# Optimization experiments

Hardware: AMD Instinct MI355X
Metric: run time of the kernel (lower is better)

## Reference

```python
import jax, jax.numpy as jnp
import numpy as np

N_EMBED = 1024
CUTOFFS = [20000, 60000, 180000]
N_VOCAB = 267735
BOUNDS = [0] + CUTOFFS + [N_VOCAB]            # cluster boundaries
N_EMBEDS = [1024, 256, 64, 16]                # n_embed / 4**i
N_TOK = 1024
N_CLUSTERS = len(CUTOFFS)                      # 3 tail clusters


def setup_inputs() -> dict:
    key = jax.random.key(0)
    ks = jax.random.split(key, 12)

    def w(k, shape):
        fan_in = shape[0]
        return (jax.random.normal(k, shape, jnp.float32) / np.sqrt(fan_in)).astype(jnp.float32)

    inp = {}
    inp["hidden"] = jax.random.normal(ks[0], (N_TOK, N_EMBED), jnp.float32)
    inp["target"] = jax.random.randint(ks[1], (N_TOK,), 0, N_VOCAB)
    # head: layers[0] = Linear(n_embed, cutoffs[0]); clusters = Linear(n_embed, n_clusters)
    inp["W_head"] = w(ks[2], (N_EMBED, BOUNDS[1]))
    inp["b_head"] = jnp.zeros((BOUNDS[1],), jnp.float32)
    inp["W_cluster"] = w(ks[3], (N_EMBED, N_CLUSTERS))
    inp["b_cluster"] = jnp.zeros((N_CLUSTERS,), jnp.float32)
    # tails: projections[i-1] = Linear(n_embed, n_embeds[i], bias=False); layers[i] = Linear(n_embeds[i], end-start)
    for i in range(1, N_CLUSTERS + 1):
        size = BOUNDS[i + 1] - BOUNDS[i]
        inp[f"W_proj{i}"] = w(ks[3 + 2 * i], (N_EMBED, N_EMBEDS[i]))
        inp[f"W_tail{i}"] = w(ks[4 + 2 * i], (N_EMBEDS[i], size))
        inp[f"b_tail{i}"] = jnp.zeros((size,), jnp.float32)
    return inp


def _adaptive_nll(hidden, target, W_head, b_head, W_cluster, b_cluster, tails):
    # head logits = [vocab cluster 0 | cluster logits], then log_softmax (matches torch.cat + log_softmax)
    head_logit = jnp.concatenate(
        [hidden @ W_head + b_head, hidden @ W_cluster + b_cluster], axis=1)  # [N, cut0 + n_clusters]
    head_lp = jax.nn.log_softmax(head_logit, axis=1)

    # cluster 0: logprob = head_lp[n, target]
    t0 = jnp.clip(target, 0, BOUNDS[1] - 1)
    lp0 = jnp.take_along_axis(head_lp, t0[:, None], axis=1)[:, 0]
    nll = jnp.where(target < BOUNDS[1], -lp0, jnp.zeros((), head_lp.dtype))

    # tail clusters i=1..3: logprob = head_lp[:, -i] + tail_log_softmax[n, target-start]
    for i, (Wp, Wt, bt) in enumerate(tails, start=1):
        start, end = BOUNDS[i], BOUNDS[i + 1]
        tail_lp = jax.nn.log_softmax((hidden @ Wp) @ Wt + bt, axis=1)  # [N, end-start]
        rel = jnp.clip(target - start, 0, end - start - 1)
        lp_i = head_lp[:, -i] + jnp.take_along_axis(tail_lp, rel[:, None], axis=1)[:, 0]
        in_bucket = (target >= start) & (target < end)
        nll = jnp.where(in_bucket, -lp_i, nll)
    return nll  # [N], per-token negative log-likelihood (keep_order=True semantics)


def reference(hidden, target, W_head, b_head, W_cluster, b_cluster,
              W_proj1, W_tail1, b_tail1,
              W_proj2, W_tail2, b_tail2,
              W_proj3, W_tail3, b_tail3):
    tails = [(W_proj1, W_tail1, b_tail1),
             (W_proj2, W_tail2, b_tail2),
             (W_proj3, W_tail3, b_tail3)]
    return _adaptive_nll(hidden, target, W_head, b_head, W_cluster, b_cluster, tails)
```

## Files before the change

kernel.cpp:

```cpp
#include <hip/hip_runtime.h>
#include <cstdint>
#include <cstddef>


typedef unsigned short u16;
typedef __attribute__((ext_vector_type(8))) __bf16 bf16x8;
typedef __attribute__((ext_vector_type(8))) u16 u16x8;
typedef __attribute__((ext_vector_type(4))) float f32x4;

#define AS1 __attribute__((address_space(1)))
#define AS3 __attribute__((address_space(3)))

__device__ __forceinline__ u16 f2bf(float f){
  union { float f; unsigned u; } v; v.f = f;
  unsigned r = v.u + 0x7fffu + ((v.u >> 16) & 1u);
  return (u16)(r >> 16);
}
__device__ __forceinline__ void glds16(const void* g, void* l){
  __builtin_amdgcn_global_load_lds((AS1 unsigned*)(uintptr_t)g,
                                   (AS3 unsigned*)(unsigned)(uintptr_t)l, 16, 0, 0);
}

__global__ void k_cvt_hidden(const float* __restrict__ h, u16* __restrict__ a0,
                             int* __restrict__ cnt, int* __restrict__ trel){
  int g = blockIdx.x * 256 + threadIdx.x;
  if (g < 4096) trel[g] = -1;
  if (g < 4) cnt[g] = 0;
  int i = g * 8;
  f32x4 v0 = *(const f32x4*)(h + i);
  f32x4 v1 = *(const f32x4*)(h + i + 4);
  u16x8 o;
  o[0]=f2bf(v0.x); o[1]=f2bf(v0.y); o[2]=f2bf(v0.z); o[3]=f2bf(v0.w);
  o[4]=f2bf(v1.x); o[5]=f2bf(v1.y); o[6]=f2bf(v1.z); o[7]=f2bf(v1.w);
  *(u16x8*)(a0 + i) = o;
}

__global__ void k_compact(const int* __restrict__ tgt, int* __restrict__ cnt,
                          int* __restrict__ idx1, int* __restrict__ idx2,
                          int* __restrict__ idx3, int* __restrict__ pos,
                          int* __restrict__ tr0, int* __restrict__ tr1,
                          int* __restrict__ tr2, int* __restrict__ tr3){
  int n = blockIdx.x * 256 + threadIdx.x;
  int t = tgt[n];
  int p = 0;
  tr0[n] = (t < 20000) ? t : -1;
  if (t >= 20000){
    int b = (t < 60000) ? 0 : (t < 180000 ? 1 : 2);
    p = atomicAdd(&cnt[b], 1);
    if (b == 0){ idx1[p] = n; tr1[p] = t - 20000; }
    else if (b == 1){ idx2[p] = n; tr2[p] = t - 60000; }
    else { idx3[p] = n; tr3[p] = t - 180000; }
  }
  pos[n] = p;
}

__global__ void k_gather(const int* __restrict__ cnt,
                         const int* __restrict__ idx1, const int* __restrict__ idx2,
                         const int* __restrict__ idx3,
                         const u16* __restrict__ A1, const u16* __restrict__ A2,
                         const u16* __restrict__ A3,
                         u16* __restrict__ A1c, u16* __restrict__ A2c,
                         u16* __restrict__ A3c){
  int u = blockIdx.x * 256 + threadIdx.x;
  const u16* src; u16* dst;
  if (u < 32768){
    int r = u >> 5, c = u & 31;
    if (r >= cnt[0]) return;
    src = A1 + (size_t)idx1[r] * 256 + c * 8;
    dst = A1c + (size_t)r * 256 + c * 8;
  } else if (u < 40960){
    int v = u - 32768; int r = v >> 3, c = v & 7;
    if (r >= cnt[1]) return;
    src = A2 + (size_t)idx2[r] * 64 + c * 8;
    dst = A2c + (size_t)r * 64 + c * 8;
  } else {
    int v = u - 40960; int r = v >> 3, c = v & 7;
    if (r >= cnt[2]) return;
    src = A3 + (size_t)idx3[r] * 64 + c * 8;
    dst = A3c + (size_t)r * 64 + c * 8;
  }
  *(u16x8*)dst = *(const u16x8*)src;
}

struct TJob { const float* W; u16* BT; int K, N, Kpad, nrows, nx, base; };
struct TJobs { TJob j[8]; int nj; };

__global__ void k_transpose_multi(TJobs jobs){
  int id = blockIdx.x;
  int ji = 0;
  #pragma unroll
  for (int i = 1; i < 8; ++i)
    if (i < jobs.nj && id >= jobs.j[i].base) ji = i;
  TJob jb = jobs.j[ji];
  int local = id - jb.base;
  int bx = local % jb.nx;
  int by = local / jb.nx;

  __shared__ float t[64][65];
  const int n0 = bx * 64;
  const int k0 = by * 64;
  const bool al = (jb.N & 3) == 0;
  for (int i = threadIdx.x; i < 64*16; i += 256){
    int r = i >> 4, c4 = (i & 15) * 4;
    int k = k0 + r, n = n0 + c4;
    f32x4 v; v.x=0.f; v.y=0.f; v.z=0.f; v.w=0.f;
    if (k < jb.K){
      if (al && n + 3 < jb.N) v = *(const f32x4*)(jb.W + (size_t)k * jb.N + n);
      else { for (int q = 0; q < 4; ++q) if (n + q < jb.N) v[q] = jb.W[(size_t)k * jb.N + n + q]; }
    }
    t[r][c4] = v.x; t[r][c4+1] = v.y; t[r][c4+2] = v.z; t[r][c4+3] = v.w;
  }
  __syncthreads();
  for (int i = threadIdx.x; i < 64*8; i += 256){
    int rn = i >> 3, c8 = (i & 7) * 8;
    if (k0 + c8 < jb.Kpad && (n0 + rn) < jb.nrows){
      u16x8 o;
      #pragma unroll
      for (int q = 0; q < 8; ++q) o[q] = f2bf(t[c8 + q][rn]);
      *(u16x8*)(jb.BT + (size_t)(n0 + rn) * jb.Kpad + k0 + c8) = o;
    }
  }
}

__global__ __launch_bounds__(512)
void k_proj_gemm(const u16* __restrict__ A, const u16* __restrict__ BT,
                 const float* __restrict__ bc,
                 u16* __restrict__ A1, u16* __restrict__ A2,
                 u16* __restrict__ A3, float* __restrict__ cl)
{
  constexpr int BK = 64, K = 1024;
  __shared__ u16 As[256 * BK];
  __shared__ u16 Bs[128 * BK];
  const int tid  = threadIdx.x;
  const int lane = tid & 63, wid = tid >> 6;
  const int wm = wid & 3, wn = wid >> 2;
  const int l15 = lane & 15, l4 = lane >> 4;
  const int m0 = blockIdx.y * 256;
  const int n0 = blockIdx.x * 128;

  f32x4 acc[4][4];
  #pragma unroll
  for (int m = 0; m < 4; ++m)
    #pragma unroll
    for (int n = 0; n < 4; ++n){ acc[m][n].x=0.f; acc[m][n].y=0.f; acc[m][n].z=0.f; acc[m][n].w=0.f; }

  for (int kt = 0; kt < K / BK; ++kt){
    #pragma unroll
    for (int i = 0; i < 4; ++i){
      int c = wid * 4 + i;
      int row = c * 8 + lane / 8, kb = lane % 8;
      glds16((const char*)(A + (size_t)(m0 + row) * K + kt * BK) + kb * 16,
             (char*)As + c * 1024);
    }
    #pragma unroll
    for (int i = 0; i < 2; ++i){
      int c = wid * 2 + i;
      int row = c * 8 + lane / 8, kb = lane % 8;
      glds16((const char*)(BT + (size_t)(n0 + row) * K + kt * BK) + kb * 16,
             (char*)Bs + c * 1024);
    }
    __syncthreads();
    #pragma unroll
    for (int ks = 0; ks < 2; ++ks){
      bf16x8 af[4], bfr[4];
      #pragma unroll
      for (int m = 0; m < 4; ++m)
        af[m] = *(const bf16x8*)((const char*)As + (wm*64 + m*16 + l15) * (BK*2) + ks*64 + l4*16);
      #pragma unroll
      for (int n = 0; n < 4; ++n)
        bfr[n] = *(const bf16x8*)((const char*)Bs + (wn*64 + n*16 + l15) * (BK*2) + ks*64 + l4*16);
      #pragma unroll
      for (int m = 0; m < 4; ++m)
        #pragma unroll
        for (int n = 0; n < 4; ++n)
          acc[m][n] = __builtin_amdgcn_mfma_f32_16x16x32_bf16(af[m], bfr[n], acc[m][n], 0, 0, 0);
    }
    __syncthreads();
  }
  #pragma unroll
  for (int m = 0; m < 4; ++m)
    #pragma unroll
    for (int n = 0; n < 4; ++n)
      #pragma unroll
      for (int q = 0; q < 4; ++q){
        int c = n0 + wn*64 + n*16 + l15;
        int r = m0 + wm*64 + m*16 + l4*4 + q;
        float v = acc[m][n][q];
        if (c < 256)      A1[(size_t)r*256 + c] = f2bf(v);
        else if (c < 320) A2[(size_t)r*64 + (c-256)] = f2bf(v);
        else if (c < 336){ u16* p = A3 + (size_t)r*64 + (c-320);
                           p[0] = f2bf(v); p[16] = 0; p[32] = 0; p[48] = 0; }
        else if (c < 339) cl[(size_t)r*3 + (c-336)] = v + bc[c-336];
      }
}

template<int BK>
__global__ __launch_bounds__(256)
void k_gemm_lse(const u16* __restrict__ A, const u16* __restrict__ BT,
                const float* __restrict__ bias, int K, int N,
                float* __restrict__ P, int ntiles,
                const int* __restrict__ cntp, int bucket,
                const int* __restrict__ tgt_rel, const int* __restrict__ rowmap,
                float* __restrict__ tl)
{
  if (cntp && (int)(blockIdx.y * 128) >= cntp[bucket]) return;
  __shared__ u16 As[128 * BK];
  __shared__ u16 Bs[128 * BK];
  __shared__ float reds[2][128];
  __shared__ int trel_s[128];

  const int tid  = threadIdx.x;
  const int lane = tid & 63, wid = tid >> 6;
  const int wm = wid & 1, wn = wid >> 1;
  const int l15 = lane & 15, l4 = lane >> 4;
  const int m0 = blockIdx.y * 128;
  const int n0 = blockIdx.x * 128;
  const int srow = lane >> 3, skb = lane & 7;

  if (tid < 128) trel_s[tid] = tgt_rel[m0 + tid];

  f32x4 acc[4][4];
  #pragma unroll
  for (int m = 0; m < 4; ++m)
    #pragma unroll
    for (int n = 0; n < 4; ++n){ acc[m][n].x=0.f; acc[m][n].y=0.f; acc[m][n].z=0.f; acc[m][n].w=0.f; }

  const int ksteps = K / BK;
  for (int kt = 0; kt < ksteps; ++kt){
    #pragma unroll
    for (int i = 0; i < 4; ++i){
      int c = wid * 4 + i;
      int row = c * 8 + srow;
      int kbs = skb ^ (row & 7);
      glds16((const char*)(A + (size_t)(m0 + row) * K + kt * BK) + kbs * 16,
             (char*)As + c * 1024);
    }
    #pragma unroll
    for (int i = 0; i < 4; ++i){
      int c = wid * 4 + i;
      int row = c * 8 + srow;
      int kbs = skb ^ (row & 7);
      glds16((const char*)(BT + (size_t)(n0 + row) * K + kt * BK) + kbs * 16,
             (char*)Bs + c * 1024);
    }
    __syncthreads();
    #pragma unroll
    for (int ks = 0; ks < 2; ++ks){
      bf16x8 af[4], bfr[4];
      #pragma unroll
      for (int m = 0; m < 4; ++m){
        int r = wm*64 + m*16 + l15;
        af[m] = *(const bf16x8*)((const char*)As + r*(BK*2) + (((ks*4 + l4) ^ (r & 7)) * 16));
      }
      #pragma unroll
      for (int n = 0; n < 4; ++n){
        int r = wn*64 + n*16 + l15;
        bfr[n] = *(const bf16x8*)((const char*)Bs + r*(BK*2) + (((ks*4 + l4) ^ (r & 7)) * 16));
      }
      #pragma unroll
      for (int m = 0; m < 4; ++m)
        #pragma unroll
        for (int n = 0; n < 4; ++n)
          acc[m][n] = __builtin_amdgcn_mfma_f32_16x16x32_bf16(af[m], bfr[n], acc[m][n], 0, 0, 0);
    }
    __syncthreads();
  }

  float bv[4]; bool val[4];
  #pragma unroll
  for (int n = 0; n < 4; ++n){
    int col = n0 + wn*64 + n*16 + l15;
    val[n] = col < N;
    bv[n] = val[n] ? bias[col] : 0.f;
  }
  #pragma unroll
  for (int m = 0; m < 4; ++m)
    #pragma unroll
    for (int q = 0; q < 4; ++q){
      int lrow = wm*64 + m*16 + l4*4 + q;
      int tr = trel_s[lrow];
      float Sl = 0.f;
      #pragma unroll
      for (int n = 0; n < 4; ++n){
        if (val[n]){
          float lg = acc[m][n][q] + bv[n];
          Sl += __expf(lg);
          int col = n0 + wn*64 + n*16 + l15;
          if (tr == col) tl[rowmap ? rowmap[m0 + lrow] : (m0 + lrow)] = lg;
        }
      }
      #pragma unroll
      for (int d = 1; d < 16; d <<= 1) Sl += __shfl_xor(Sl, d);
      if (l15 == 0) reds[wn][lrow] = Sl;
    }
  __syncthreads();
  if (wn == 0 && l15 == 0){
    #pragma unroll
    for (int m = 0; m < 4; ++m)
      #pragma unroll
      for (int q = 0; q < 4; ++q){
        int lrow = wm*64 + m*16 + l4*4 + q;
        P[(size_t)(m0 + lrow) * ntiles + blockIdx.x] = reds[0][lrow] + reds[1][lrow];
      }
  }
}

template<int NC>
__global__ __launch_bounds__(256)
void k_gemm_lse_s(const u16* __restrict__ A, const u16* __restrict__ BT,
                  const float* __restrict__ bias, int N,
                  float* __restrict__ P, int ntiles,
                  const int* __restrict__ cntp, int bucket,
                  const int* __restrict__ tgt_rel, const int* __restrict__ rowmap,
                  float* __restrict__ tl)
{
  constexpr int BK = 64;
  const int m0 = blockIdx.y * 128;
  if (m0 >= cntp[bucket]) return;
  const int cg = blockIdx.x;

  __shared__ u16 As[128 * BK];
  __shared__ u16 Bs[2][128 * BK];
  __shared__ float reds[2][128];
  __shared__ int trel_s[128];

  const int tid  = threadIdx.x;
  const int lane = tid & 63, wid = tid >> 6;
  const int wm = wid & 1, wn = wid >> 1;
  const int l15 = lane & 15, l4 = lane >> 4;
  const int srow = lane >> 3, skb = lane & 7;

  if (tid < 128) trel_s[tid] = tgt_rel[m0 + tid];

  #pragma unroll
  for (int i = 0; i < 4; ++i){
    int c = wid * 4 + i;
    int row = c * 8 + srow;
    int kbs = skb ^ (row & 7);
    glds16((const char*)(A + (size_t)(m0 + row) * BK) + kbs * 16,
           (char*)As + c * 1024);
  }
  {
    int ci0 = cg * NC;
    if (ci0 < ntiles){
      #pragma unroll
      for (int i = 0; i < 4; ++i){
        int c = wid * 4 + i;
        int row = c * 8 + srow;
        int kbs = skb ^ (row & 7);
        glds16((const char*)(BT + (size_t)(ci0*128 + row) * BK) + kbs * 16,
               (char*)Bs[0] + c * 1024);
      }
    }
  }
  __syncthreads();

  int buf = 0;
  for (int ct = 0; ct < NC; ++ct){
    int ci = cg * NC + ct;
    if (ci >= ntiles) break;
    if (ct + 1 < NC && ci + 1 < ntiles){
      #pragma unroll
      for (int i = 0; i < 4; ++i){
        int c = wid * 4 + i;
        int row = c * 8 + srow;
        int kbs = skb ^ (row & 7);
        glds16((const char*)(BT + (size_t)((ci+1)*128 + row) * BK) + kbs * 16,
               (char*)Bs[buf ^ 1] + c * 1024);
      }
    }
    f32x4 acc[4][4];
    #pragma unroll
    for (int m = 0; m < 4; ++m)
      #pragma unroll
      for (int n = 0; n < 4; ++n){ acc[m][n].x=0.f; acc[m][n].y=0.f; acc[m][n].z=0.f; acc[m][n].w=0.f; }
    #pragma unroll
    for (int ks = 0; ks < 2; ++ks){
      bf16x8 af[4], bfr[4];
      #pragma unroll
      for (int m = 0; m < 4; ++m){
        int r = wm*64 + m*16 + l15;
        af[m] = *(const bf16x8*)((const char*)As + r*(BK*2) + (((ks*4 + l4) ^ (r & 7)) * 16));
      }
      #pragma unroll
      for (int n = 0; n < 4; ++n){
        int r = wn*64 + n*16 + l15;
        bfr[n] = *(const bf16x8*)((const char*)Bs[buf] + r*(BK*2) + (((ks*4 + l4) ^ (r & 7)) * 16));
      }
      #pragma unroll
      for (int m = 0; m < 4; ++m)
        #pragma unroll
        for (int n = 0; n < 4; ++n)
          acc[m][n] = __builtin_amdgcn_mfma_f32_16x16x32_bf16(af[m], bfr[n], acc[m][n], 0, 0, 0);
    }
    const int n0 = ci * 128;
    float bv[4]; bool val[4];
    #pragma unroll
    for (int n = 0; n < 4; ++n){
      int col = n0 + wn*64 + n*16 + l15;
      val[n] = col < N;
      bv[n] = val[n] ? bias[col] : 0.f;
    }
    #pragma unroll
    for (int m = 0; m < 4; ++m)
      #pragma unroll
      for (int q = 0; q < 4; ++q){
        int lrow = wm*64 + m*16 + l4*4 + q;
        int tr = trel_s[lrow];
        float Sl = 0.f;
        #pragma unroll
        for (int n = 0; n < 4; ++n){
          if (val[n]){
            float lg = acc[m][n][q] + bv[n];
            Sl += __expf(lg);
            int col = n0 + wn*64 + n*16 + l15;
            if (tr == col) tl[rowmap[m0 + lrow]] = lg;
          }
        }
        #pragma unroll
        for (int d = 1; d < 16; d <<= 1) Sl += __shfl_xor(Sl, d);
        if (l15 == 0) reds[wn][lrow] = Sl;
      }
    __syncthreads();
    if (wn == 0 && l15 == 0){
      #pragma unroll
      for (int m = 0; m < 4; ++m)
        #pragma unroll
        for (int q = 0; q < 4; ++q){
          int lrow = wm*64 + m*16 + l4*4 + q;
          P[(size_t)(m0 + lrow) * ntiles + ci] = reds[0][lrow] + reds[1][lrow];
        }
    }
    __syncthreads();
    buf ^= 1;
  }
}

__global__ void k_finalize(const int* __restrict__ tgt, const float* __restrict__ P,
                           const float* __restrict__ cl, const float* __restrict__ tl,
                           const int* __restrict__ pos, float* __restrict__ out)
{
  const int NT0 = 157, NT1 = 313, NT2 = 938, NT3 = 686;
  int n = blockIdx.x * 4 + (threadIdx.x >> 6);
  int lane = threadIdx.x & 63;
  int t = tgt[n];

  float s = 0.f;
  const float* p0 = P + (size_t)n * NT0;
  for (int i = lane; i < NT0; i += 64) s += p0[i];
  if (lane < 3) s += __expf(cl[n*3 + lane]);
  #pragma unroll
  for (int d = 1; d < 64; d <<= 1) s += __shfl_xor(s, d);
  float lse_head = logf(s);

  float nll;
  if (t < 20000){
    nll = lse_head - tl[n];
  } else {
    int seg, nt; size_t base;
    if      (t <  60000){ seg = 1; nt = NT1; base = (size_t)1024 * NT0; }
    else if (t < 180000){ seg = 2; nt = NT2; base = (size_t)1024 * (NT0 + NT1); }
    else                { seg = 3; nt = NT3; base = (size_t)1024 * (NT0 + NT1 + NT2); }
    float s2 = 0.f;
    const float* ps = P + base + (size_t)pos[n] * nt;
    for (int i = lane; i < nt; i += 64) s2 += ps[i];
    #pragma unroll
    for (int d = 1; d < 64; d <<= 1) s2 += __shfl_xor(s2, d);
    float lse_t = logf(s2);
    nll = lse_head - cl[n*3 + (3 - seg)] + lse_t - tl[n];
  }
  if (lane == 0) out[n] = nll;
}

extern "C" void kernel_launch(void* const* d_in, const int* in_sizes, int n_in,
                              void* d_out, int out_size, void* d_ws, size_t ws_size,
                              hipStream_t stream)
{
  const float* hidden = (const float*)d_in[0];
  const int*   target = (const int*)d_in[1];
  const float* W_head = (const float*)d_in[2];
  const float* b_head = (const float*)d_in[3];
  const float* W_clu  = (const float*)d_in[4];
  const float* b_clu  = (const float*)d_in[5];
  const float* W_p1   = (const float*)d_in[6];
  const float* W_t1   = (const float*)d_in[7];
  const float* b_t1   = (const float*)d_in[8];
  const float* W_p2   = (const float*)d_in[9];
  const float* W_t2   = (const float*)d_in[10];
  const float* b_t2   = (const float*)d_in[11];
  const float* W_p3   = (const float*)d_in[12];
  const float* W_t3   = (const float*)d_in[13];
  const float* b_t3   = (const float*)d_in[14];
  float* out = (float*)d_out;

  char* ws = (char*)d_ws;
  u16*   A0  = (u16*)(ws + 0);
  u16*   A1  = (u16*)(ws + 2097152);
  u16*   A2  = (u16*)(ws + 2621440);
  u16*   A3  = (u16*)(ws + 2752512);
  float* cl  = (float*)(ws + 2883584);
  float* tl  = (float*)(ws + 2895872);
  float* P   = (float*)(ws + 2899968);
  u16*   BTp = (u16*)(ws + 2899968);
  u16*   BTh = (u16*)(ws + 11476992);
  int*   cnt  = (int*)(ws + 52633600);
  int*   idx1 = (int*)(ws + 52633856);
  int*   idx2 = (int*)(ws + 52637952);
  int*   idx3 = (int*)(ws + 52642048);
  int*   pos  = (int*)(ws + 52646144);
  u16*   A1c  = (u16*)(ws + 52650240);
  u16*   A2c  = (u16*)(ws + 53174528);
  u16*   A3c  = (u16*)(ws + 53305600);
  int*   tr0  = (int*)(ws + 53436672);
  int*   tr1  = (int*)(ws + 53440768);
  int*   tr2  = (int*)(ws + 53444864);
  int*   tr3  = (int*)(ws + 53448960);
  u16*   BT1  = (u16*)(ws + 53453056);
  u16*   BT2  = (u16*)(ws + 73965824);
  u16*   BT3  = (u16*)(ws + 89334016);
  const size_t needA = 100573440;
  const bool bigws = ws_size >= needA;

  float* P0  = P;
  float* Pp1 = P + (size_t)1024 * 157;
  float* Pp2 = P + (size_t)1024 * (157 + 313);
  float* Pp3 = P + (size_t)1024 * (157 + 313 + 938);

  k_cvt_hidden<<<512, 256, 0, stream>>>(hidden, A0, cnt, tr0);
  k_compact<<<4, 256, 0, stream>>>(target, cnt, idx1, idx2, idx3, pos,
                                   tr0, tr1, tr2, tr3);

  TJobs tj{}; int nb = 0;
  auto add = [&](const float* W, u16* B, int K, int N, int Kpad, int nrows){
    int nx = (nrows + 63) / 64;
    int ny = (Kpad + 63) / 64;
    tj.j[tj.nj++] = TJob{W, B, K, N, Kpad, nrows, nx, nb};
    nb += nx * ny;
  };
  add(W_p1, BTp, 1024, 256, 1024, 256);
  add(W_p2, BTp + (size_t)256*1024, 1024, 64, 1024, 64);
  add(W_p3, BTp + (size_t)320*1024, 1024, 16, 1024, 16);
  add(W_clu, BTp + (size_t)336*1024, 1024, 3, 1024, 64);
  add(W_head, BTh, 1024, 20000, 1024, 20096);
  if (bigws){
    add(W_t1, BT1, 256, 40000, 256, 40064);
    add(W_t2, BT2, 64, 120000, 64, 120064);
    add(W_t3, BT3, 16, 87735, 64, 87808);
  }
  k_transpose_multi<<<nb, 256, 0, stream>>>(tj);

  k_proj_gemm<<<dim3(3, 4), 512, 0, stream>>>(A0, BTp, b_clu, A1, A2, A3, cl);
  k_gather<<<192, 256, 0, stream>>>(cnt, idx1, idx2, idx3, A1, A2, A3, A1c, A2c, A3c);

  k_gemm_lse<64><<<dim3(157, 8), 256, 0, stream>>>(A0, BTh, b_head, 1024, 20000,
      P0, 157, nullptr, 0, tr0, nullptr, tl);

  if (bigws){
    k_gemm_lse<64><<<dim3(313, 8), 256, 0, stream>>>(A1c, BT1, b_t1, 256, 40000,
        Pp1, 313, cnt, 0, tr1, idx1, tl);
    k_gemm_lse_s<4><<<dim3(235, 8), 256, 0, stream>>>(A2c, BT2, b_t2, 120000,
        Pp2, 938, cnt, 1, tr2, idx2, tl);
    k_gemm_lse_s<4><<<dim3(172, 8), 256, 0, stream>>>(A3c, BT3, b_t3, 87735,
        Pp3, 686, cnt, 2, tr3, idx3, tl);
  } else {
    TJobs s1{}; s1.nj = 1; s1.j[0] = TJob{W_t1, BTh, 256, 40000, 256, 40064, 626, 0};
    k_transpose_multi<<<626*4, 256, 0, stream>>>(s1);
    k_gemm_lse<64><<<dim3(313, 8), 256, 0, stream>>>(A1c, BTh, b_t1, 256, 40000,
        Pp1, 313, cnt, 0, tr1, idx1, tl);
    TJobs s2{}; s2.nj = 1; s2.j[0] = TJob{W_t2, BTh, 64, 120000, 64, 120064, 1876, 0};
    k_transpose_multi<<<1876, 256, 0, stream>>>(s2);
    k_gemm_lse_s<4><<<dim3(235, 8), 256, 0, stream>>>(A2c, BTh, b_t2, 120000,
        Pp2, 938, cnt, 1, tr2, idx2, tl);
    TJobs s3{}; s3.nj = 1; s3.j[0] = TJob{W_t3, BTh, 16, 87735, 64, 87808, 1372, 0};
    k_transpose_multi<<<1372, 256, 0, stream>>>(s3);
    k_gemm_lse_s<4><<<dim3(172, 8), 256, 0, stream>>>(A3c, BTh, b_t3, 87735,
        Pp3, 686, cnt, 2, tr3, idx3, tl);
  }

  k_finalize<<<256, 256, 0, stream>>>(target, P, cl, tl, pos, out);
}
```

Baseline: 305.9 us.

## Store head and tail1 weights in blocked tiles and shrink tail3 K padding

The transpose kernel can now write the bf16 transposed weights in a tiled layout of 128 rows by 64 K, so the head and tail-1 GEMMs read each B tile as one contiguous 16KB chunk instead of 128 strided rows. Tail-3 activations and weights are padded to K=32 instead of 64, and the small-K GEMM is templated on BK with matching swizzle and load counts. This halves the padded work and bandwidth for cluster 3. The workspace threshold is lowered, which relies on the buffer offsets still fitting.

```diff
diff --git a/kernel.cpp b/kernel.cpp
--- a/kernel.cpp
+++ b/kernel.cpp
@@ -74,15 +74,15 @@
     src = A2 + (size_t)idx2[r] * 64 + c * 8;
     dst = A2c + (size_t)r * 64 + c * 8;
   } else {
-    int v = u - 40960; int r = v >> 3, c = v & 7;
+    int v = u - 40960; int r = v >> 2, c = v & 3;
     if (r >= cnt[2]) return;
-    src = A3 + (size_t)idx3[r] * 64 + c * 8;
-    dst = A3c + (size_t)r * 64 + c * 8;
+    src = A3 + (size_t)idx3[r] * 32 + c * 8;
+    dst = A3c + (size_t)r * 32 + c * 8;
   }
   *(u16x8*)dst = *(const u16x8*)src;
 }
 
-struct TJob { const float* W; u16* BT; int K, N, Kpad, nrows, nx, base; };
+struct TJob { const float* W; u16* BT; int K, N, Kpad, nrows, nx, base, blk; };
 struct TJobs { TJob j[8]; int nj; };
 
 __global__ void k_transpose_multi(TJobs jobs){
@@ -113,11 +113,17 @@
   __syncthreads();
   for (int i = threadIdx.x; i < 64*8; i += 256){
     int rn = i >> 3, c8 = (i & 7) * 8;
-    if (k0 + c8 < jb.Kpad && (n0 + rn) < jb.nrows){
+    int n = n0 + rn;
+    if (k0 + c8 < jb.Kpad && n < jb.nrows){
       u16x8 o;
       #pragma unroll
       for (int q = 0; q < 8; ++q) o[q] = f2bf(t[c8 + q][rn]);
-      *(u16x8*)(jb.BT + (size_t)(n0 + rn) * jb.Kpad + k0 + c8) = o;
+      size_t off;
+      if (jb.blk)
+        off = (((size_t)(n >> 7) * (jb.Kpad >> 6) + (k0 >> 6)) * 128 + (n & 127)) * 64 + c8;
+      else
+        off = (size_t)n * jb.Kpad + k0 + c8;
+      *(u16x8*)(jb.BT + off) = o;
     }
   }
 }
@@ -188,13 +194,13 @@
         float v = acc[m][n][q];
         if (c < 256)      A1[(size_t)r*256 + c] = f2bf(v);
         else if (c < 320) A2[(size_t)r*64 + (c-256)] = f2bf(v);
-        else if (c < 336){ u16* p = A3 + (size_t)r*64 + (c-320);
-                           p[0] = f2bf(v); p[16] = 0; p[32] = 0; p[48] = 0; }
+        else if (c < 336){ u16* p = A3 + (size_t)r*32 + (c-320);
+                           p[0] = f2bf(v); p[16] = 0; }
         else if (c < 339) cl[(size_t)r*3 + (c-336)] = v + bc[c-336];
       }
 }
 
-template<int BK>
+template<int BK, bool BLK>
 __global__ __launch_bounds__(256)
 void k_gemm_lse(const u16* __restrict__ A, const u16* __restrict__ BT,
                 const float* __restrict__ bias, int K, int N,
@@ -240,8 +246,12 @@
       int c = wid * 4 + i;
       int row = c * 8 + srow;
       int kbs = skb ^ (row & 7);
-      glds16((const char*)(BT + (size_t)(n0 + row) * K + kt * BK) + kbs * 16,
-             (char*)Bs + c * 1024);
+      const char* src;
+      if (BLK)
+        src = (const char*)(BT + ((size_t)(blockIdx.x * ksteps + kt) * 128 + row) * 64);
+      else
+        src = (const char*)(BT + (size_t)(n0 + row) * K + kt * BK);
+      glds16(src + kbs * 16, (char*)Bs + c * 1024);
     }
     __syncthreads();
     #pragma unroll
@@ -305,7 +315,7 @@
   }
 }
 
-template<int NC>
+template<int NC, int BK>
 __global__ __launch_bounds__(256)
 void k_gemm_lse_s(const u16* __restrict__ A, const u16* __restrict__ BT,
                   const float* __restrict__ bias, int N,
@@ -314,7 +324,10 @@
                   const int* __restrict__ tgt_rel, const int* __restrict__ rowmap,
                   float* __restrict__ tl)
 {
-  constexpr int BK = 64;
+  constexpr int CH  = BK / 8;
+  constexpr int LPR = CH;
+  constexpr int RPC = 64 / LPR;
+  constexpr int CPW = (128 * BK * 2 / 1024) / 4;
   const int m0 = blockIdx.y * 128;
   if (m0 >= cntp[bucket]) return;
   const int cg = blockIdx.x;
@@ -328,15 +341,15 @@
   const int lane = tid & 63, wid = tid >> 6;
   const int wm = wid & 1, wn = wid >> 1;
   const int l15 = lane & 15, l4 = lane >> 4;
-  const int srow = lane >> 3, skb = lane & 7;
+  const int srow = lane / LPR, skb = lane % LPR;
 
   if (tid < 128) trel_s[tid] = tgt_rel[m0 + tid];
 
   #pragma unroll
-  for (int i = 0; i < 4; ++i){
-    int c = wid * 4 + i;
-    int row = c * 8 + srow;
-    int kbs = skb ^ (row & 7);
+  for (int i = 0; i < CPW; ++i){
+    int c = wid * CPW + i;
+    int row = c * RPC + srow;
+    int kbs = skb ^ (row & (CH - 1));
     glds16((const char*)(A + (size_t)(m0 + row) * BK) + kbs * 16,
            (char*)As + c * 1024);
   }
@@ -344,10 +357,10 @@
     int ci0 = cg * NC;
     if (ci0 < ntiles){
       #pragma unroll
-      for (int i = 0; i < 4; ++i){
-        int c = wid * 4 + i;
-        int row = c * 8 + srow;
-        int kbs = skb ^ (row & 7);
+      for (int i = 0; i < CPW; ++i){
+        int c = wid * CPW + i;
+        int row = c * RPC + srow;
+        int kbs = skb ^ (row & (CH - 1));
         glds16((const char*)(BT + (size_t)(ci0*128 + row) * BK) + kbs * 16,
                (char*)Bs[0] + c * 1024);
       }
@@ -361,10 +374,10 @@
     if (ci >= ntiles) break;
     if (ct + 1 < NC && ci + 1 < ntiles){
       #pragma unroll
-      for (int i = 0; i < 4; ++i){
-        int c = wid * 4 + i;
-        int row = c * 8 + srow;
-        int kbs = skb ^ (row & 7);
+      for (int i = 0; i < CPW; ++i){
+        int c = wid * CPW + i;
+        int row = c * RPC + srow;
+        int kbs = skb ^ (row & (CH - 1));
         glds16((const char*)(BT + (size_t)((ci+1)*128 + row) * BK) + kbs * 16,
                (char*)Bs[buf ^ 1] + c * 1024);
       }
@@ -375,17 +388,17 @@
       #pragma unroll
       for (int n = 0; n < 4; ++n){ acc[m][n].x=0.f; acc[m][n].y=0.f; acc[m][n].z=0.f; acc[m][n].w=0.f; }
     #pragma unroll
-    for (int ks = 0; ks < 2; ++ks){
+    for (int ks = 0; ks < BK / 32; ++ks){
       bf16x8 af[4], bfr[4];
       #pragma unroll
       for (int m = 0; m < 4; ++m){
         int r = wm*64 + m*16 + l15;
-        af[m] = *(const bf16x8*)((const char*)As + r*(BK*2) + (((ks*4 + l4) ^ (r & 7)) * 16));
+        af[m] = *(const bf16x8*)((const char*)As + r*(BK*2) + (((ks*4 + l4) ^ (r & (CH-1))) * 16));
       }
       #pragma unroll
       for (int n = 0; n < 4; ++n){
         int r = wn*64 + n*16 + l15;
-        bfr[n] = *(const bf16x8*)((const char*)Bs[buf] + r*(BK*2) + (((ks*4 + l4) ^ (r & 7)) * 16));
+        bfr[n] = *(const bf16x8*)((const char*)Bs[buf] + r*(BK*2) + (((ks*4 + l4) ^ (r & (CH-1))) * 16));
       }
       #pragma unroll
       for (int m = 0; m < 4; ++m)
@@ -518,7 +531,7 @@
   u16*   BT1  = (u16*)(ws + 53453056);
   u16*   BT2  = (u16*)(ws + 73965824);
   u16*   BT3  = (u16*)(ws + 89334016);
-  const size_t needA = 100573440;
+  const size_t needA = 95000000;
   const bool bigws = ws_size >= needA;
 
   float* P0  = P;
@@ -531,49 +544,49 @@
                                    tr0, tr1, tr2, tr3);
 
   TJobs tj{}; int nb = 0;
-  auto add = [&](const float* W, u16* B, int K, int N, int Kpad, int nrows){
+  auto add = [&](const float* W, u16* B, int K, int N, int Kpad, int nrows, int blk){
     int nx = (nrows + 63) / 64;
     int ny = (Kpad + 63) / 64;
-    tj.j[tj.nj++] = TJob{W, B, K, N, Kpad, nrows, nx, nb};
+    tj.j[tj.nj++] = TJob{W, B, K, N, Kpad, nrows, nx, nb, blk};
     nb += nx * ny;
   };
-  add(W_p1, BTp, 1024, 256, 1024, 256);
-  add(W_p2, BTp + (size_t)256*1024, 1024, 64, 1024, 64);
-  add(W_p3, BTp + (size_t)320*1024, 1024, 16, 1024, 16);
-  add(W_clu, BTp + (size_t)336*1024, 1024, 3, 1024, 64);
-  add(W_head, BTh, 1024, 20000, 1024, 20096);
+  add(W_p1, BTp, 1024, 256, 1024, 256, 0);
+  add(W_p2, BTp + (size_t)256*1024, 1024, 64, 1024, 64, 0);
+  add(W_p3, BTp + (size_t)320*1024, 1024, 16, 1024, 16, 0);
+  add(W_clu, BTp + (size_t)336*1024, 1024, 3, 1024, 64, 0);
+  add(W_head, BTh, 1024, 20000, 1024, 20096, 1);
   if (bigws){
-    add(W_t1, BT1, 256, 40000, 256, 40064);
-    add(W_t2, BT2, 64, 120000, 64, 120064);
-    add(W_t3, BT3, 16, 87735, 64, 87808);
+    add(W_t1, BT1, 256, 40000, 256, 40064, 1);
+    add(W_t2, BT2, 64, 120000, 64, 120064, 0);
+    add(W_t3, BT3, 16, 87735, 32, 87808, 0);
   }
   k_transpose_multi<<<nb, 256, 0, stream>>>(tj);
 
   k_proj_gemm<<<dim3(3, 4), 512, 0, stream>>>(A0, BTp, b_clu, A1, A2, A3, cl);
   k_gather<<<192, 256, 0, stream>>>(cnt, idx1, idx2, idx3, A1, A2, A3, A1c, A2c, A3c);
 
-  k_gemm_lse<64><<<dim3(157, 8), 256, 0, stream>>>(A0, BTh, b_head, 1024, 20000,
+  k_gemm_lse<64, true><<<dim3(157, 8), 256, 0, stream>>>(A0, BTh, b_head, 1024, 20000,
       P0, 157, nullptr, 0, tr0, nullptr, tl);
 
   if (bigws){
-    k_gemm_lse<64><<<dim3(313, 8), 256, 0, stream>>>(A1c, BT1, b_t1, 256, 40000,
+    k_gemm_lse<64, true><<<dim3(313, 8), 256, 0, stream>>>(A1c, BT1, b_t1, 256, 40000,
         Pp1, 313, cnt, 0, tr1, idx1, tl);
-    k_gemm_lse_s<4><<<dim3(235, 8), 256, 0, stream>>>(A2c, BT2, b_t2, 120000,
+    k_gemm_lse_s<4, 64><<<dim3(235, 8), 256, 0, stream>>>(A2c, BT2, b_t2, 120000,
         Pp2, 938, cnt, 1, tr2, idx2, tl);
-    k_gemm_lse_s<4><<<dim3(172, 8), 256, 0, stream>>>(A3c, BT3, b_t3, 87735,
+    k_gemm_lse_s<4, 32><<<dim3(172, 8), 256, 0, stream>>>(A3c, BT3, b_t3, 87735,
         Pp3, 686, cnt, 2, tr3, idx3, tl);
   } else {
-    TJobs s1{}; s1.nj = 1; s1.j[0] = TJob{W_t1, BTh, 256, 40000, 256, 40064, 626, 0};
+    TJobs s1{}; s1.nj = 1; s1.j[0] = TJob{W_t1, BTh, 256, 40000, 256, 40064, 626, 0, 1};
     k_transpose_multi<<<626*4, 256, 0, stream>>>(s1);
-    k_gemm_lse<64><<<dim3(313, 8), 256, 0, stream>>>(A1c, BTh, b_t1, 256, 40000,
+    k_gemm_lse<64, true><<<dim3(313, 8), 256, 0, stream>>>(A1c, BTh, b_t1, 256, 40000,
         Pp1, 313, cnt, 0, tr1, idx1, tl);
-    TJobs s2{}; s2.nj = 1; s2.j[0] = TJob{W_t2, BTh, 64, 120000, 64, 120064, 1876, 0};
+    TJobs s2{}; s2.nj = 1; s2.j[0] = TJob{W_t2, BTh, 64, 120000, 64, 120064, 1876, 0, 0};
     k_transpose_multi<<<1876, 256, 0, stream>>>(s2);
-    k_gemm_lse_s<4><<<dim3(235, 8), 256, 0, stream>>>(A2c, BTh, b_t2, 120000,
+    k_gemm_lse_s<4, 64><<<dim3(235, 8), 256, 0, stream>>>(A2c, BTh, b_t2, 120000,
         Pp2, 938, cnt, 1, tr2, idx2, tl);
-    TJobs s3{}; s3.nj = 1; s3.j[0] = TJob{W_t3, BTh, 16, 87735, 64, 87808, 1372, 0};
+    TJobs s3{}; s3.nj = 1; s3.j[0] = TJob{W_t3, BTh, 16, 87735, 32, 87808, 1372, 0, 0};
     k_transpose_multi<<<1372, 256, 0, stream>>>(s3);
-    k_gemm_lse_s<4><<<dim3(172, 8), 256, 0, stream>>>(A3c, BTh, b_t3, 87735,
+    k_gemm_lse_s<4, 32><<<dim3(172, 8), 256, 0, stream>>>(A3c, BTh, b_t3, 87735,
         Pp3, 686, cnt, 2, tr3, idx3, tl);
   }
 
```

New measurement: 277.4 us. -9.3%, faster.
